# Kernel tuning notes

Measured on AMD Instinct MI355X. Metric: run time of the kernel, lower is better.

Reference implementation:

```python
import jax, jax.numpy as jnp
import numpy as np

B, S, H, E = 4, 2048, 2048, 8

def _gelu(x):
    return jax.nn.gelu(x, approximate=False)  # torch nn.GELU default (erf)

def setup_inputs() -> dict:
    key = jax.random.key(0)
    ks = jax.random.split(key, 12)
    sc = 1.0 / np.sqrt(H)
    inp = {
        'hidden_states': jax.random.normal(ks[0], (B, S, H), jnp.float32),
        'attention_mask': jnp.ones((B, S), jnp.float32),
        # operation detector: Linear(H,H) -> GELU -> Linear(H,8)
        'Wd1': jax.random.normal(ks[1], (H, H), jnp.float32) * sc,
        'bd1': jnp.zeros((H,), jnp.float32),
        'Wd2': jax.random.normal(ks[2], (H, E), jnp.float32) * sc,
        'bd2': jnp.zeros((E,), jnp.float32),
        # 8 expert handlers, each PrecisionAdaptiveLinear(H,H) -> stacked [E,H,H]
        'We': jax.random.normal(ks[3], (E, H, H), jnp.float32) * sc,
        'be': jnp.zeros((E, H), jnp.float32),
        # precision_integration: Linear(H,H) -> GELU -> Linear(H,H)
        'Wi1': jax.random.normal(ks[4], (H, H), jnp.float32) * sc,
        'bi1': jnp.zeros((H,), jnp.float32),
        'Wi2': jax.random.normal(ks[5], (H, H), jnp.float32) * sc,
        'bi2': jnp.zeros((H,), jnp.float32),
    }
    return inp

def _kahan_sum_last(x):
    # Numerically-stable Kahan summation over the last axis (E elements).
    s = jnp.zeros_like(x[..., 0])
    c = jnp.zeros_like(s)
    for i in range(x.shape[-1]):
        y = x[..., i] - c
        t = s + y
        c = (t - s) - y
        s = t
    return s

def reference(hidden_states, attention_mask, Wd1, bd1, Wd2, bd2, We, be, Wi1, bi1, Wi2, bi2):
    h = hidden_states
    # router: softmax over 8 operation logits (safe_softmax == stable softmax)
    logits = _gelu(h @ Wd1 + bd1) @ Wd2 + bd2            # [B,S,E]
    op_w = jax.nn.softmax(logits, axis=-1)               # [B,S,E]
    # all 8 expert linears as one batched GEMM: [B,S,E,H]
    expert_out = jnp.einsum('bsh,ehk->bsek', h, We) + be
    weighted = expert_out * op_w[:, :, :, None]          # [B,S,E,H]
    # Kahan-combine over experts (move E to last axis)
    combined = _kahan_sum_last(jnp.moveaxis(weighted, 2, -1))  # [B,S,H]
    enhanced = _gelu(combined @ Wi1 + bi1) @ Wi2 + bi2   # [B,S,H]
    enhanced = enhanced * attention_mask[:, :, None]
    return enhanced
```

## Files before the change

kernel.cpp:

```cpp
#include <hip/hip_runtime.h>
#include <hip/hip_bf16.h>


#define MTOT 8192
#define HDIM 2048
#define WMAT ((size_t)HDIM * HDIM)

typedef short bf16x8 __attribute__((ext_vector_type(8)));
typedef float f32x4  __attribute__((ext_vector_type(4)));
typedef unsigned short u16;

__device__ __forceinline__ u16 f2bf(float x) {
    unsigned int u = __float_as_uint(x);
    return (u16)((u + 0x7FFFu + ((u >> 16) & 1u)) >> 16);
}
__device__ __forceinline__ float bf2f(u16 u) {
    return __uint_as_float(((unsigned int)u) << 16);
}
__device__ __forceinline__ float gelu_f(float x) {
    return 0.5f * x * (1.0f + erff(x * 0.70710678118654752f));
}

__global__ void k_split_x(const float* __restrict__ x,
                          u16* __restrict__ hi, u16* __restrict__ lo, long n) {
    long i = ((long)blockIdx.x * blockDim.x + threadIdx.x) * 4;
    long stride = (long)gridDim.x * blockDim.x * 4;
    for (; i < n; i += stride) {
        float4 v = *reinterpret_cast<const float4*>(x + i);
        ushort4 h, l;
        h.x = f2bf(v.x); l.x = f2bf(v.x - bf2f(h.x));
        h.y = f2bf(v.y); l.y = f2bf(v.y - bf2f(h.y));
        h.z = f2bf(v.z); l.z = f2bf(v.z - bf2f(h.z));
        h.w = f2bf(v.w); l.w = f2bf(v.w - bf2f(h.w));
        *reinterpret_cast<ushort4*>(hi + i) = h;
        *reinterpret_cast<ushort4*>(lo + i) = l;
    }
}

__global__ void k_split_tr(const float* __restrict__ Wd1, const float* __restrict__ We,
                           const float* __restrict__ Wi1, const float* __restrict__ Wi2,
                           u16* __restrict__ th, u16* __restrict__ tl) {
    int z = blockIdx.z;
    const float* src = (z == 0) ? Wd1
                     : (z <= 8) ? (We + (size_t)(z - 1) * WMAT)
                     : (z == 9) ? Wi1 : Wi2;
    size_t dof = (size_t)z * WMAT;
    __shared__ float t[32][33];
    int n0 = blockIdx.x * 32, k0 = blockIdx.y * 32;
    int tx = threadIdx.x & 31, ty = threadIdx.x >> 5;
#pragma unroll
    for (int i = 0; i < 4; ++i) {
        int k = ty + i * 8;
        t[k][tx] = src[(size_t)(k0 + k) * HDIM + n0 + tx];
    }
    __syncthreads();
#pragma unroll
    for (int i = 0; i < 4; ++i) {
        int n = ty + i * 8;
        float v = t[tx][n];
        u16 hv = f2bf(v), lv = f2bf(v - bf2f(hv));
        th[dof + (size_t)(n0 + n) * HDIM + k0 + tx] = hv;
        tl[dof + (size_t)(n0 + n) * HDIM + k0 + tx] = lv;
    }
}

__global__ void k_logits(const float* __restrict__ G1, const float* __restrict__ Wd2,
                         const float* __restrict__ bd2, float* __restrict__ opw) {
    int row = blockIdx.x * (blockDim.x >> 6) + (threadIdx.x >> 6);
    int lane = threadIdx.x & 63;
    if (row >= MTOT) return;
    const float* g = G1 + (size_t)row * HDIM;
    float a[8] = {0, 0, 0, 0, 0, 0, 0, 0};
    for (int k = lane; k < HDIM; k += 64) {
        float x = g[k];
        const float* w = Wd2 + (size_t)k * 8;
        float4 w0 = *reinterpret_cast<const float4*>(w);
        float4 w1 = *reinterpret_cast<const float4*>(w + 4);
        a[0] += x * w0.x; a[1] += x * w0.y; a[2] += x * w0.z; a[3] += x * w0.w;
        a[4] += x * w1.x; a[5] += x * w1.y; a[6] += x * w1.z; a[7] += x * w1.w;
    }
#pragma unroll
    for (int off = 32; off > 0; off >>= 1)
#pragma unroll
        for (int e = 0; e < 8; ++e) a[e] += __shfl_xor(a[e], off);
#pragma unroll
    for (int e = 0; e < 8; ++e) a[e] += bd2[e];
    float mx = a[0];
#pragma unroll
    for (int e = 1; e < 8; ++e) mx = fmaxf(mx, a[e]);
    float p[8], s = 0.f;
#pragma unroll
    for (int e = 0; e < 8; ++e) { p[e] = expf(a[e] - mx); s += p[e]; }
    float inv = 1.f / s;
    if (lane < 8) opw[(size_t)row * 8 + lane] = p[lane] * inv;
}

__device__ __forceinline__ void stage_tile32(const u16* __restrict__ g, size_t row0,
                                             int k0, u16* dst, int tid) {
    int wv = tid >> 6;
#pragma unroll
    for (int i = 0; i < 2; ++i) {
        int slot = i * 512 + tid;
        int row = slot >> 2, chunk = slot & 3;
        const u16* src = g + (row0 + (size_t)row) * HDIM + k0 + chunk * 8;
        u16* d = dst + (size_t)((i * 512 + wv * 64) << 3);
        __builtin_amdgcn_global_load_lds((const __attribute__((address_space(1))) void*)src,
                                         (__attribute__((address_space(3))) void*)d,
                                         16, 0, 0);
    }
}

template <int NE, int EPI>
__global__ __launch_bounds__(512, 2)
void k_mm(const u16* __restrict__ Ah, const u16* __restrict__ Al,
          const u16* __restrict__ Bh, const u16* __restrict__ Bl,
          const float* __restrict__ opw, const float* __restrict__ bias,
          const float* __restrict__ mask, float* __restrict__ outF,
          u16* __restrict__ oHi, u16* __restrict__ oLo) {
    __shared__ u16 lsA[2][2][256 * 32];
    __shared__ u16 lsB[2][2][256 * 32];
    __shared__ float rat[NE == 8 ? 256 * 8 : 8];

    const int tid = threadIdx.x, lane = tid & 63, wv = tid >> 6;
    const int bx = blockIdx.x & 7, by = blockIdx.x >> 3;
    const size_t row0 = (size_t)by * 256, col0 = (size_t)bx * 256;
    const int wm = wv >> 1, wn = wv & 1;
    const int lp = lane & 15, lq = lane >> 4;

    if (NE == 8 && tid < 256) {
        const float* w = opw + (row0 + tid) * 8;
        float w8[8];
#pragma unroll
        for (int e = 0; e < 8; ++e) w8[e] = w[e];
#pragma unroll
        for (int e = 0; e < 8; ++e) rat[tid * 8 + e] = w8[(e + 7) & 7] / w8[e];
    }

    stage_tile32(Ah, row0, 0, lsA[0][0], tid);
    stage_tile32(Al, row0, 0, lsA[0][1], tid);
    stage_tile32(Bh, col0, 0, lsB[0][0], tid);
    stage_tile32(Bl, col0, 0, lsB[0][1], tid);
    __syncthreads();

    f32x4 acc[4][8] = {};
    const int NS = NE * (HDIM / 32);
    int ab = 0, bb = 0;

    for (int s = 0; s < NS; ++s) {
        const int e = s & (NE - 1);
        const int s1 = s + 1;
        if (s1 < NS) {
            const int e1 = s1 & (NE - 1);
            const int k1 = (s1 / NE) * 32;
            if (e1 == 0) {
                stage_tile32(Ah, row0, k1, lsA[ab ^ 1][0], tid);
                stage_tile32(Al, row0, k1, lsA[ab ^ 1][1], tid);
            }
            stage_tile32(Bh + (size_t)e1 * WMAT, col0, k1, lsB[bb ^ 1][0], tid);
            stage_tile32(Bl + (size_t)e1 * WMAT, col0, k1, lsB[bb ^ 1][1], tid);
        }
        if (NE == 8 && s > 0) {
#pragma unroll
            for (int m = 0; m < 4; ++m)
#pragma unroll
                for (int r = 0; r < 4; ++r) {
                    float rv = rat[(wm * 64 + m * 16 + lq * 4 + r) * 8 + e];
#pragma unroll
                    for (int n = 0; n < 8; ++n) acc[m][n][r] *= rv;
                }
        }
        bf16x8 fah[4], fal[4];
#pragma unroll
        for (int m = 0; m < 4; ++m) {
            int rr = wm * 64 + m * 16 + lp;
            fah[m] = *(const bf16x8*)(lsA[ab][0] + rr * 32 + lq * 8);
            fal[m] = *(const bf16x8*)(lsA[ab][1] + rr * 32 + lq * 8);
        }
#pragma unroll
        for (int n = 0; n < 8; ++n) {
            int cr = wn * 128 + n * 16 + lp;
            bf16x8 fbh = *(const bf16x8*)(lsB[bb][0] + cr * 32 + lq * 8);
            bf16x8 fbl = *(const bf16x8*)(lsB[bb][1] + cr * 32 + lq * 8);
#pragma unroll
            for (int m = 0; m < 4; ++m) {
                acc[m][n] = __builtin_amdgcn_mfma_f32_16x16x32_bf16(fah[m], fbh, acc[m][n], 0, 0, 0);
                acc[m][n] = __builtin_amdgcn_mfma_f32_16x16x32_bf16(fah[m], fbl, acc[m][n], 0, 0, 0);
                acc[m][n] = __builtin_amdgcn_mfma_f32_16x16x32_bf16(fal[m], fbh, acc[m][n], 0, 0, 0);
            }
        }
        __syncthreads();
        if (s1 < NS) {
            if ((s1 & (NE - 1)) == 0) ab ^= 1;
            bb ^= 1;
        }
    }

    if constexpr (EPI == 1) {
        float bev[8][8];
#pragma unroll
        for (int n = 0; n < 8; ++n) {
            size_t gc = col0 + wn * 128 + n * 16 + lp;
#pragma unroll
            for (int e = 0; e < 8; ++e) bev[n][e] = bias[(size_t)e * HDIM + gc];
        }
#pragma unroll
        for (int m = 0; m < 4; ++m)
#pragma unroll
            for (int r = 0; r < 4; ++r) {
                size_t gr = row0 + wm * 64 + m * 16 + lq * 4 + r;
                const float* w = opw + gr * 8;
                float w8[8];
#pragma unroll
                for (int e = 0; e < 8; ++e) w8[e] = w[e];
#pragma unroll
                for (int n = 0; n < 8; ++n) {
                    float bsum = 0.f;
#pragma unroll
                    for (int e = 0; e < 8; ++e) bsum += w8[e] * bev[n][e];
                    float v = acc[m][n][r] * w8[7] + bsum;
                    size_t gc = col0 + wn * 128 + n * 16 + lp;
                    u16 hv = f2bf(v), lv = f2bf(v - bf2f(hv));
                    oHi[gr * HDIM + gc] = hv;
                    oLo[gr * HDIM + gc] = lv;
                }
            }
    } else {
#pragma unroll
        for (int n = 0; n < 8; ++n) {
            size_t gc = col0 + wn * 128 + n * 16 + lp;
            float bv = bias[gc];
#pragma unroll
            for (int m = 0; m < 4; ++m)
#pragma unroll
                for (int r = 0; r < 4; ++r) {
                    size_t gr = row0 + wm * 64 + m * 16 + lq * 4 + r;
                    float v = acc[m][n][r] + bv;
                    if constexpr (EPI == 0) {
                        outF[gr * HDIM + gc] = gelu_f(v);
                    } else if constexpr (EPI == 2) {
                        v = gelu_f(v);
                        u16 hv = f2bf(v), lv = f2bf(v - bf2f(hv));
                        oHi[gr * HDIM + gc] = hv;
                        oLo[gr * HDIM + gc] = lv;
                    } else {
                        outF[gr * HDIM + gc] = v * mask[gr];
                    }
                }
        }
    }
}

extern "C" void kernel_launch(void* const* d_in, const int* in_sizes, int n_in,
                              void* d_out, int out_size, void* d_ws, size_t ws_size,
                              hipStream_t stream) {
    const float* h    = (const float*)d_in[0];
    const float* amsk = (const float*)d_in[1];
    const float* Wd1  = (const float*)d_in[2];
    const float* bd1  = (const float*)d_in[3];
    const float* Wd2  = (const float*)d_in[4];
    const float* bd2  = (const float*)d_in[5];
    const float* We   = (const float*)d_in[6];
    const float* be   = (const float*)d_in[7];
    const float* Wi1  = (const float*)d_in[8];
    const float* bi1  = (const float*)d_in[9];
    const float* Wi2  = (const float*)d_in[10];
    const float* bi2  = (const float*)d_in[11];
    float* out = (float*)d_out;

    const size_t MB = 1ull << 20;
    char* ws = (char*)d_ws;
    u16* Xh = (u16*)(ws);
    u16* Xl = (u16*)(ws + 32 * MB);
    u16* Wth = (u16*)(ws + 64 * MB);
    u16* Wtl = (u16*)(ws + 152 * MB);
    char* rc = ws + 240 * MB;
    float* G1  = (float*)rc;
    u16*   Chi = (u16*)rc;
    u16*   Clo = (u16*)(rc + 32 * MB);
    float* opw = (float*)(ws + 304 * MB);
    u16* Thi = Xh;
    u16* Tlo = Xl;

    k_split_x<<<4096, 256, 0, stream>>>(h, Xh, Xl, (long)MTOT * HDIM);
    k_split_tr<<<dim3(64, 64, 11), 256, 0, stream>>>(Wd1, We, Wi1, Wi2, Wth, Wtl);

    k_mm<1, 0><<<256, 512, 0, stream>>>(Xh, Xl, Wth, Wtl, nullptr, bd1, nullptr,
                                        G1, nullptr, nullptr);
    k_logits<<<MTOT / 4, 256, 0, stream>>>(G1, Wd2, bd2, opw);
    k_mm<8, 1><<<256, 512, 0, stream>>>(Xh, Xl, Wth + WMAT, Wtl + WMAT, opw, be,
                                        nullptr, nullptr, Chi, Clo);
    k_mm<1, 2><<<256, 512, 0, stream>>>(Chi, Clo, Wth + 9 * WMAT, Wtl + 9 * WMAT,
                                        nullptr, bi1, nullptr, nullptr, Thi, Tlo);
    k_mm<1, 3><<<256, 512, 0, stream>>>(Thi, Tlo, Wth + 10 * WMAT, Wtl + 10 * WMAT,
                                        nullptr, bi2, amsk, out, nullptr, nullptr);
}
```

Before: 2.441 ms.

## Interleave hi/lo bf16 tiles in LDS with XOR swizzle and raise MFMA priority

The separate hi and lo LDS tile buffers are merged into one 64-element-wide row per tile, with an XOR swizzle on 16-byte chunks applied both when staging via global_load_lds and when reading fragments. This is meant to cut LDS bank conflicts on the fragment reads and halve the number of staging calls. It also wraps the MFMA inner loop in s_setprio(1)/s_setprio(0) so the matrix-core instruction stream is favoured over other waves' memory work. The swizzle must agree exactly between the write and read paths, and the priority hint may change interleaving with loads in ways that are hard to predict.

```diff
diff --git a/kernel.cpp b/kernel.cpp
--- a/kernel.cpp
+++ b/kernel.cpp
@@ -95,19 +95,27 @@
     if (lane < 8) opw[(size_t)row * 8 + lane] = p[lane] * inv;
 }
 
-__device__ __forceinline__ void stage_tile32(const u16* __restrict__ g, size_t row0,
-                                             int k0, u16* dst, int tid) {
+__device__ __forceinline__ void stage_fused(const u16* __restrict__ gh,
+                                            const u16* __restrict__ gl,
+                                            size_t row0, int k0, u16* dst, int tid) {
     int wv = tid >> 6;
 #pragma unroll
-    for (int i = 0; i < 2; ++i) {
+    for (int i = 0; i < 4; ++i) {
         int slot = i * 512 + tid;
-        int row = slot >> 2, chunk = slot & 3;
-        const u16* src = g + (row0 + (size_t)row) * HDIM + k0 + chunk * 8;
-        u16* d = dst + (size_t)((i * 512 + wv * 64) << 3);
+        int row = slot >> 3, p = slot & 7;
+        int l = p ^ (row & 7);
+        const u16* base = (l < 4) ? gh : gl;
+        const u16* src = base + (row0 + (size_t)row) * HDIM + k0 + (l & 3) * 8;
+        u16* d = dst + ((size_t)(i * 512 + wv * 64) << 3);
         __builtin_amdgcn_global_load_lds((const __attribute__((address_space(1))) void*)src,
                                          (__attribute__((address_space(3))) void*)d,
                                          16, 0, 0);
     }
+}
+
+__device__ __forceinline__ bf16x8 rd_f(const u16* t, int r, int l) {
+    int p = l ^ (r & 7);
+    return *reinterpret_cast<const bf16x8*>(t + (size_t)r * 64 + p * 8);
 }
 
 template <int NE, int EPI>
@@ -117,8 +125,8 @@
           const float* __restrict__ opw, const float* __restrict__ bias,
           const float* __restrict__ mask, float* __restrict__ outF,
           u16* __restrict__ oHi, u16* __restrict__ oLo) {
-    __shared__ u16 lsA[2][2][256 * 32];
-    __shared__ u16 lsB[2][2][256 * 32];
+    __shared__ u16 lsA[2][256 * 64];
+    __shared__ u16 lsB[2][256 * 64];
     __shared__ float rat[NE == 8 ? 256 * 8 : 8];
 
     const int tid = threadIdx.x, lane = tid & 63, wv = tid >> 6;
@@ -136,10 +144,8 @@
         for (int e = 0; e < 8; ++e) rat[tid * 8 + e] = w8[(e + 7) & 7] / w8[e];
     }
 
-    stage_tile32(Ah, row0, 0, lsA[0][0], tid);
-    stage_tile32(Al, row0, 0, lsA[0][1], tid);
-    stage_tile32(Bh, col0, 0, lsB[0][0], tid);
-    stage_tile32(Bl, col0, 0, lsB[0][1], tid);
+    stage_fused(Ah, Al, row0, 0, lsA[0], tid);
+    stage_fused(Bh, Bl, col0, 0, lsB[0], tid);
     __syncthreads();
 
     f32x4 acc[4][8] = {};
@@ -152,12 +158,10 @@
         if (s1 < NS) {
             const int e1 = s1 & (NE - 1);
             const int k1 = (s1 / NE) * 32;
-            if (e1 == 0) {
-                stage_tile32(Ah, row0, k1, lsA[ab ^ 1][0], tid);
-                stage_tile32(Al, row0, k1, lsA[ab ^ 1][1], tid);
-            }
-            stage_tile32(Bh + (size_t)e1 * WMAT, col0, k1, lsB[bb ^ 1][0], tid);
-            stage_tile32(Bl + (size_t)e1 * WMAT, col0, k1, lsB[bb ^ 1][1], tid);
+            if (e1 == 0)
+                stage_fused(Ah, Al, row0, k1, lsA[ab ^ 1], tid);
+            stage_fused(Bh + (size_t)e1 * WMAT, Bl + (size_t)e1 * WMAT,
+                        col0, k1, lsB[bb ^ 1], tid);
         }
         if (NE == 8 && s > 0) {
 #pragma unroll
@@ -173,20 +177,22 @@
 #pragma unroll
         for (int m = 0; m < 4; ++m) {
             int rr = wm * 64 + m * 16 + lp;
-            fah[m] = *(const bf16x8*)(lsA[ab][0] + rr * 32 + lq * 8);
-            fal[m] = *(const bf16x8*)(lsA[ab][1] + rr * 32 + lq * 8);
+            fah[m] = rd_f(lsA[ab], rr, lq);
+            fal[m] = rd_f(lsA[ab], rr, 4 + lq);
         }
 #pragma unroll
         for (int n = 0; n < 8; ++n) {
             int cr = wn * 128 + n * 16 + lp;
-            bf16x8 fbh = *(const bf16x8*)(lsB[bb][0] + cr * 32 + lq * 8);
-            bf16x8 fbl = *(const bf16x8*)(lsB[bb][1] + cr * 32 + lq * 8);
+            bf16x8 fbh = rd_f(lsB[bb], cr, lq);
+            bf16x8 fbl = rd_f(lsB[bb], cr, 4 + lq);
+            __builtin_amdgcn_s_setprio(1);
 #pragma unroll
             for (int m = 0; m < 4; ++m) {
                 acc[m][n] = __builtin_amdgcn_mfma_f32_16x16x32_bf16(fah[m], fbh, acc[m][n], 0, 0, 0);
                 acc[m][n] = __builtin_amdgcn_mfma_f32_16x16x32_bf16(fah[m], fbl, acc[m][n], 0, 0, 0);
                 acc[m][n] = __builtin_amdgcn_mfma_f32_16x16x32_bf16(fal[m], fbh, acc[m][n], 0, 0, 0);
             }
+            __builtin_amdgcn_s_setprio(0);
         }
         __syncthreads();
         if (s1 < NS) {
```

Measured after the change: 2.472 ms. Within noise of the previous version (+1.2%).
